# Performance work log

Hardware: AMD Instinct MI355X
Metric: run time of the kernel (lower is better)

The kernel has to match this reference:

```python
import jax, jax.numpy as jnp
import numpy as np

N, E, D, H = 100000, 400000, 128, 128  # nodes, edges, feat dim, mlp hidden


def _ln(x, g, b, eps=1e-5):
    m = jnp.mean(x, axis=-1, keepdims=True)
    v = jnp.mean((x - m) ** 2, axis=-1, keepdims=True)
    return (x - m) * jax.lax.rsqrt(v + eps) * g + b


def _mlp(x, w0, b0, w1, b1, w2, b2):
    # Linear->ReLU->Linear->ReLU->Linear (last act = Identity)
    h = jax.nn.relu(x @ w0 + b0)
    h = jax.nn.relu(h @ w1 + b1)
    return h @ w2 + b2


def setup_inputs() -> dict:
    key = jax.random.key(0)
    ks = jax.random.split(key, 16)
    node_x = jax.random.normal(ks[0], (N, D), dtype=jnp.float32)
    edge_attr = jax.random.normal(ks[1], (E, D), dtype=jnp.float32)
    edge_index = jax.random.randint(ks[2], (2, E), 0, N, dtype=jnp.int32)

    def lin(k, fin, fout):
        kw, kb = jax.random.split(k)
        s = 1.0 / np.sqrt(fin)
        w = jax.random.uniform(kw, (fin, fout), jnp.float32, -s, s)
        b = jax.random.uniform(kb, (fout,), jnp.float32, -s, s)
        return w, b

    # message MLP: (3D) -> H -> H -> D, then LayerNorm(D)
    msg_w0, msg_b0 = lin(ks[3], 3 * D, H)
    msg_w1, msg_b1 = lin(ks[4], H, H)
    msg_w2, msg_b2 = lin(ks[5], H, D)
    # top-level update MLP: (D + D) -> H -> H -> D, then LayerNorm(D)
    upd_w0, upd_b0 = lin(ks[6], 2 * D, H)
    upd_w1, upd_b1 = lin(ks[7], H, H)
    upd_w2, upd_b2 = lin(ks[8], H, D)
    return {
        "node_x": node_x, "edge_attr": edge_attr, "edge_index": edge_index,
        "msg_w0": msg_w0, "msg_b0": msg_b0, "msg_w1": msg_w1, "msg_b1": msg_b1,
        "msg_w2": msg_w2, "msg_b2": msg_b2,
        "msg_g": jnp.ones((D,), jnp.float32), "msg_beta": jnp.zeros((D,), jnp.float32),
        "upd_w0": upd_w0, "upd_b0": upd_b0, "upd_w1": upd_w1, "upd_b1": upd_b1,
        "upd_w2": upd_w2, "upd_b2": upd_b2,
        "upd_g": jnp.ones((D,), jnp.float32), "upd_beta": jnp.zeros((D,), jnp.float32),
    }


def reference(node_x, edge_attr, edge_index,
              msg_w0, msg_b0, msg_w1, msg_b1, msg_w2, msg_b2, msg_g, msg_beta,
              upd_w0, upd_b0, upd_w1, upd_b1, upd_w2, upd_b2, upd_g, upd_beta):
    src, dst = edge_index[0], edge_index[1]
    # PyG default flow source_to_target: x_j = x[src], x_i = x[dst]
    x_i = node_x[dst]                       # [E, D]
    x_j = node_x[src]                       # [E, D]
    concat = jnp.concatenate([x_i, x_j, edge_attr], axis=1)  # [E, 3D]
    msg = _ln(_mlp(concat, msg_w0, msg_b0, msg_w1, msg_b1, msg_w2, msg_b2), msg_g, msg_beta)
    new_edge = edge_attr + msg              # edge_attr[:] += msg in original
    # scatter-add messages onto target nodes
    agg = jax.ops.segment_sum(new_edge, dst, num_segments=N)  # [N, D]
    concat2 = jnp.concatenate([node_x, agg], axis=1)          # [N, 2D]
    upd = _ln(_mlp(concat2, upd_w0, upd_b0, upd_w1, upd_b1, upd_w2, upd_b2), upd_g, upd_beta)
    return node_x + upd
```

## Files before the change

### kernel.cpp

```cpp
#include <hip/hip_runtime.h>

typedef __attribute__((ext_vector_type(4))) float f32x4;
typedef __attribute__((ext_vector_type(8))) __bf16 bf16x8;

constexpr int FD = 128;

__device__ __forceinline__ uint4 pack8(const float* v) {
  union { __bf16 h[8]; uint4 u; } cv;
#pragma unroll
  for (int q = 0; q < 8; ++q) cv.h[q] = (__bf16)v[q];
  return cv.u;
}
__device__ __forceinline__ unsigned int pack2(float a, float b) {
  union { __bf16 h[2]; unsigned int u; } cv;
  cv.h[0] = (__bf16)a; cv.h[1] = (__bf16)b;
  return cv.u;
}

__global__ void cvt_bf16(const float* __restrict__ x, unsigned short* __restrict__ o, int n8) {
  int i = blockIdx.x * 256 + threadIdx.x;
  if (i >= n8) return;
  const float* p = x + (size_t)i * 8;
  float v[8];
#pragma unroll
  for (int q = 0; q < 8; ++q) v[q] = p[q];
  *(uint4*)(o + (size_t)i * 8) = pack8(v);
}

__global__ void pack_weights(const float* __restrict__ mw0, const float* __restrict__ mw1,
                             const float* __restrict__ mw2, const float* __restrict__ uw0,
                             const float* __restrict__ uw1, const float* __restrict__ uw2,
                             unsigned short* __restrict__ wp) {
  int tid = blockIdx.x * 256 + threadIdx.x;
  const float* src; int base, K;
  if      (tid < 49152)  { src = mw0; base = 0;      K = 384; }
  else if (tid < 65536)  { src = mw1; base = 49152;  K = 128; }
  else if (tid < 81920)  { src = mw2; base = 65536;  K = 128; }
  else if (tid < 114688) { src = uw0; base = 81920;  K = 256; }
  else if (tid < 131072) { src = uw1; base = 114688; K = 128; }
  else                   { src = uw2; base = 131072; K = 128; }
  int i = tid - base;
  int k = i >> 7, n = i & 127;
  int KS = K >> 5;
  int dst = base + (((n >> 4) * KS + (k >> 5)) * 64 + ((k >> 3) & 3) * 16 + (n & 15)) * 8 + (k & 7);
  union { __bf16 h; unsigned short s; } cv; cv.h = (__bf16)src[i];
  wp[dst] = cv.s;
}


template<bool RELU>
__device__ __forceinline__ void store_frag(unsigned short* sDst, const f32x4* acc, float bias) {
#pragma unroll
  for (int m = 0; m < 4; ++m)
#pragma unroll
    for (int ri = 0; ri < 4; ++ri) {
      float v = acc[m][ri] + bias;
      if (RELU) v = fmaxf(v, 0.f);
      union { __bf16 h; unsigned short s; } cv; cv.h = (__bf16)v;
      sDst[m * 512 + ri * 32] = cv.s;
    }
}

__global__ __launch_bounds__(512, 6)
void in_edge_kernel(const float* __restrict__ node_x, const unsigned short* __restrict__ nxbf,
                    const float* __restrict__ edge_attr,
                    const int* __restrict__ eidx, const unsigned short* __restrict__ wp,
                    const float* __restrict__ b0p, const float* __restrict__ b1p,
                    const float* __restrict__ b2p, const float* __restrict__ gp,
                    const float* __restrict__ bep,
                    unsigned short* __restrict__ msg, int* __restrict__ head,
                    int* __restrict__ nxt, float* __restrict__ agg,
                    int use_sort, int E) {
  __shared__ unsigned short sBuf[3072 * 8];
  __shared__ int sSrc[64], sDst[64];
  __shared__ float sG[128], sB[128];

  const int t = threadIdx.x;
  const int e0 = blockIdx.x * 64;
  const int lane = t & 63, w = t >> 6;
  const int ln = lane & 15, g16 = lane >> 4;
  const int col = w * 16 + ln;
  const int rdoff = ln * 32 + g16 * 8;
  const int stoff = (w >> 1) * 2048 + g16 * 128
                  + (((2 * w) + (ln >> 3)) & 3) * 8 + (ln & 7);

  bf16x8 b0[6];
#pragma unroll
  for (int ks = 0; ks < 6; ++ks)
    b0[ks] = *(const bf16x8*)(wp + (size_t)((w * 12 + ks) * 64 + lane) * 8);
  bf16x8 B1r[4];
#pragma unroll
  for (int ks = 0; ks < 4; ++ks)
    B1r[ks] = *(const bf16x8*)(wp + 49152 + (size_t)((w * 4 + ks) * 64 + lane) * 8);

  if (t < 64) {
    sSrc[t] = (e0 + t < E) ? eidx[e0 + t] : 0;
  } else if (t < 128) {
    int r = t - 64;
    int e = e0 + r;
    int d = (e < E) ? eidx[E + e] : 0;
    sDst[r] = d;
    if (use_sort && e < E) nxt[e] = atomicExch(&head[d], e);
  } else if (t < 256) {
    sG[t - 128] = gp[t - 128];
  } else if (t < 384) {
    sB[t - 256] = bep[t - 256];
  }
  __syncthreads();

  if (nxbf) {
#pragma unroll
    for (int it = 0; it < 2; ++it) {
      int f = t + it * 512;
      int row = f >> 4, j = f & 15;
      uint4 v = {0, 0, 0, 0}, u = {0, 0, 0, 0};
      if (e0 + row < E) {
        v = *(const uint4*)(nxbf + (size_t)sDst[row] * FD + j * 8);
        u = *(const uint4*)(nxbf + (size_t)sSrc[row] * FD + j * 8);
      }
      int c = (((j >> 2) * 4 + (row >> 4)) * 64 + (row & 15) * 4 + (j & 3)) * 8;
      *(uint4*)&sBuf[c] = v;
      *(uint4*)&sBuf[c + 8192] = u;
    }
  } else {
#pragma unroll
    for (int it = 0; it < 16; ++it) {
      const int type = it >> 3;
      int row = ((it & 7) << 3) + w;
      float2 v = {0.f, 0.f};
      if (e0 + row < E) {
        const float* sp = (type == 0) ? node_x + (size_t)sDst[row] * FD
                                      : node_x + (size_t)sSrc[row] * FD;
        v = *(const float2*)(sp + lane * 2);
      }
      int c = (((type * 4 + (lane >> 4)) * 4 + (row >> 4)) * 64
               + (row & 15) * 4 + ((lane >> 2) & 3)) * 8 + (lane & 3) * 2;
      *(unsigned int*)&sBuf[c] = pack2(v.x, v.y);
    }
  }
#pragma unroll
  for (int it = 0; it < 8; ++it) {
    int row = it * 8 + w;
    float2 v = {0.f, 0.f};
    if (e0 + row < E) v = *(const float2*)(edge_attr + (size_t)(e0 + row) * FD + lane * 2);
    int c = 16384 + (((lane >> 4) * 4 + (row >> 4)) * 64
                     + (row & 15) * 4 + ((lane >> 2) & 3)) * 8 + (lane & 3) * 2;
    *(unsigned int*)&sBuf[c] = pack2(v.x, v.y);
  }
  __syncthreads();

  const float b0v = b0p[col], b1v = b1p[col], b2v = b2p[col];

  f32x4 acc[4];
#pragma unroll
  for (int m = 0; m < 4; ++m) acc[m] = (f32x4){0.f, 0.f, 0.f, 0.f};

#pragma unroll
  for (int ks = 0; ks < 12; ++ks) {
    bf16x8 bb = b0[ks % 6];
    if (ks + 6 < 12)
      b0[ks % 6] = *(const bf16x8*)(wp + (size_t)((w * 12 + ks + 6) * 64 + lane) * 8);
#pragma unroll
    for (int m = 0; m < 4; ++m) {
      bf16x8 a = *(const bf16x8*)&sBuf[(ks * 4 + m) * 512 + rdoff];
      acc[m] = __builtin_amdgcn_mfma_f32_16x16x32_bf16(a, bb, acc[m], 0, 0, 0);
    }
  }
  bf16x8 B2r[4];
#pragma unroll
  for (int ks = 0; ks < 4; ++ks)
    B2r[ks] = *(const bf16x8*)(wp + 65536 + (size_t)((w * 4 + ks) * 64 + lane) * 8);

  __syncthreads();
  store_frag<true>(sBuf + stoff, acc, b0v);
  __syncthreads();

#pragma unroll
  for (int m = 0; m < 4; ++m) acc[m] = (f32x4){0.f, 0.f, 0.f, 0.f};
#pragma unroll
  for (int ks = 0; ks < 4; ++ks)
#pragma unroll
    for (int m = 0; m < 4; ++m) {
      bf16x8 a = *(const bf16x8*)&sBuf[(ks * 4 + m) * 512 + rdoff];
      acc[m] = __builtin_amdgcn_mfma_f32_16x16x32_bf16(a, B1r[ks], acc[m], 0, 0, 0);
    }
  store_frag<true>(sBuf + 8192 + stoff, acc, b1v);
  __syncthreads();

#pragma unroll
  for (int m = 0; m < 4; ++m) acc[m] = (f32x4){0.f, 0.f, 0.f, 0.f};
#pragma unroll
  for (int ks = 0; ks < 4; ++ks)
#pragma unroll
    for (int m = 0; m < 4; ++m) {
      bf16x8 a = *(const bf16x8*)&sBuf[8192 + (ks * 4 + m) * 512 + rdoff];
      acc[m] = __builtin_amdgcn_mfma_f32_16x16x32_bf16(a, B2r[ks], acc[m], 0, 0, 0);
    }
  store_frag<false>(sBuf + stoff, acc, b2v);
  __syncthreads();

  {
    int row = t >> 3, j = t & 7;
    int a0 = (((j >> 1) * 4 + (row >> 4)) * 64 + (row & 15) * 4 + 2 * (j & 1)) * 8;
    bf16x8 v0 = *(const bf16x8*)&sBuf[a0];
    bf16x8 v1 = *(const bf16x8*)&sBuf[a0 + 8];
    float s1 = 0.f, s2 = 0.f;
#pragma unroll
    for (int q = 0; q < 8; ++q) {
      float a = (float)v0[q], b = (float)v1[q];
      s1 += a + b; s2 += a * a + b * b;
    }
#pragma unroll
    for (int m = 1; m < 8; m <<= 1) {
      s1 += __shfl_xor(s1, m, 64);
      s2 += __shfl_xor(s2, m, 64);
    }
    float mean = s1 * (1.f / 128.f);
    float var  = s2 * (1.f / 128.f) - mean * mean;
    float rstd = rsqrtf(fmaxf(var, 0.f) + 1e-5f);

    int e = e0 + row;
    if (e < E) {
      bf16x8 ea0 = *(const bf16x8*)&sBuf[a0 + 16384];
      bf16x8 ea1 = *(const bf16x8*)&sBuf[a0 + 16384 + 8];
      float val[16];
#pragma unroll
      for (int q = 0; q < 8; ++q) {
        val[q]     = ((float)v0[q] - mean) * rstd * sG[j * 16 + q]     + sB[j * 16 + q]     + (float)ea0[q];
        val[8 + q] = ((float)v1[q] - mean) * rstd * sG[j * 16 + 8 + q] + sB[j * 16 + 8 + q] + (float)ea1[q];
      }
      if (use_sort) {
        uint4* dst = (uint4*)(msg + (size_t)e * FD + j * 16);
        dst[0] = pack8(val);
        dst[1] = pack8(val + 8);
      } else {
        float* ap = agg + (size_t)sDst[row] * FD + j * 16;
#pragma unroll
        for (int q = 0; q < 16; ++q) atomicAdd(ap + q, val[q]);
      }
    }
  }
}

__global__ __launch_bounds__(512, 8)
void in_node_kernel(const float* __restrict__ node_x, const unsigned short* __restrict__ nxbf,
                    const unsigned short* __restrict__ msg, const int* __restrict__ head,
                    const int* __restrict__ nxt, const float* __restrict__ agg,
                    const unsigned short* __restrict__ wp,
                    const float* __restrict__ b0p, const float* __restrict__ b1p,
                    const float* __restrict__ b2p, const float* __restrict__ gp,
                    const float* __restrict__ bep, float* __restrict__ out,
                    int use_sort, int N) {
  __shared__ unsigned short sBuf[2048 * 8];
  __shared__ float sG[128], sB[128];

  const int t = threadIdx.x;
  const int r0 = blockIdx.x * 64;
  const int lane = t & 63, w = t >> 6;
  const int ln = lane & 15, g16 = lane >> 4;
  const int col = w * 16 + ln;
  const int rdoff = ln * 32 + g16 * 8;
  const int stoff = (w >> 1) * 2048 + g16 * 128
                  + (((2 * w) + (ln >> 3)) & 3) * 8 + (ln & 7);

  bf16x8 b0[4];
#pragma unroll
  for (int ks = 0; ks < 4; ++ks)
    b0[ks] = *(const bf16x8*)(wp + 81920 + (size_t)((w * 8 + ks) * 64 + lane) * 8);

  if (t < 128)      sG[t] = gp[t];
  else if (t < 256) sB[t - 128] = bep[t - 128];

  if (nxbf) {
#pragma unroll
    for (int it = 0; it < 2; ++it) {
      int f = t + it * 512;
      int row = f >> 4, j = f & 15;
      int r = r0 + row;
      uint4 v = {0, 0, 0, 0};
      if (r < N) v = *(const uint4*)(nxbf + (size_t)r * FD + j * 8);
      int c = (((j >> 2) * 4 + (row >> 4)) * 64 + (row & 15) * 4 + (j & 3)) * 8;
      *(uint4*)&sBuf[c] = v;
    }
  } else {
#pragma unroll
    for (int it = 0; it < 8; ++it) {
      int row = (it << 3) + w;
      int r = r0 + row;
      float2 v = {0.f, 0.f};
      if (r < N) v = *(const float2*)(node_x + (size_t)r * FD + lane * 2);
      int c = (((lane >> 4) * 4 + (row >> 4)) * 64
               + (row & 15) * 4 + ((lane >> 2) & 3)) * 8 + (lane & 3) * 2;
      *(unsigned int*)&sBuf[c] = pack2(v.x, v.y);
    }
  }

  {
    int row = t >> 3, j = t & 7;
    int node = r0 + row;
    float a[16];
#pragma unroll
    for (int q = 0; q < 16; ++q) a[q] = 0.f;
    if (node < N) {
      if (use_sort) {
        int e = head[node];
        while (e >= 0) {
          int ne = nxt[e];
          bf16x8 m0 = *(const bf16x8*)(msg + (size_t)e * FD + j * 16);
          bf16x8 m1 = *(const bf16x8*)(msg + (size_t)e * FD + j * 16 + 8);
#pragma unroll
          for (int q = 0; q < 8; ++q) { a[q] += (float)m0[q]; a[8 + q] += (float)m1[q]; }
          e = ne;
        }
      } else {
        const float* ap = agg + (size_t)node * FD + j * 16;
#pragma unroll
        for (int q4 = 0; q4 < 4; ++q4) {
          f32x4 u = *(const f32x4*)(ap + q4 * 4);
#pragma unroll
          for (int q = 0; q < 4; ++q) a[q4 * 4 + q] = u[q];
        }
      }
    }
    int c = 8192 + (((j >> 1) * 4 + (row >> 4)) * 64 + (row & 15) * 4 + 2 * (j & 1)) * 8;
    *(uint4*)&sBuf[c] = pack8(a);
    *(uint4*)&sBuf[c + 8] = pack8(a + 8);
  }
  __syncthreads();

  const float b0v = b0p[col], b1v = b1p[col], b2v = b2p[col];

  f32x4 acc[4];
#pragma unroll
  for (int m = 0; m < 4; ++m) acc[m] = (f32x4){0.f, 0.f, 0.f, 0.f};

#pragma unroll
  for (int ks = 0; ks < 8; ++ks) {
    bf16x8 bb = b0[ks % 4];
    if (ks + 4 < 8)
      b0[ks % 4] = *(const bf16x8*)(wp + 81920 + (size_t)((w * 8 + ks + 4) * 64 + lane) * 8);
#pragma unroll
    for (int m = 0; m < 4; ++m) {
      bf16x8 a = *(const bf16x8*)&sBuf[(ks * 4 + m) * 512 + rdoff];
      acc[m] = __builtin_amdgcn_mfma_f32_16x16x32_bf16(a, bb, acc[m], 0, 0, 0);
    }
  }
  bf16x8 B1r[4];
#pragma unroll
  for (int ks = 0; ks < 4; ++ks)
    B1r[ks] = *(const bf16x8*)(wp + 114688 + (size_t)((w * 4 + ks) * 64 + lane) * 8);

  __syncthreads();
  store_frag<true>(sBuf + stoff, acc, b0v);
  __syncthreads();

#pragma unroll
  for (int m = 0; m < 4; ++m) acc[m] = (f32x4){0.f, 0.f, 0.f, 0.f};
#pragma unroll
  for (int ks = 0; ks < 4; ++ks)
#pragma unroll
    for (int m = 0; m < 4; ++m) {
      bf16x8 a = *(const bf16x8*)&sBuf[(ks * 4 + m) * 512 + rdoff];
      acc[m] = __builtin_amdgcn_mfma_f32_16x16x32_bf16(a, B1r[ks], acc[m], 0, 0, 0);
    }
  bf16x8 B2r[4];
#pragma unroll
  for (int ks = 0; ks < 4; ++ks)
    B2r[ks] = *(const bf16x8*)(wp + 131072 + (size_t)((w * 4 + ks) * 64 + lane) * 8);
  store_frag<true>(sBuf + 8192 + stoff, acc, b1v);
  __syncthreads();

#pragma unroll
  for (int m = 0; m < 4; ++m) acc[m] = (f32x4){0.f, 0.f, 0.f, 0.f};
#pragma unroll
  for (int ks = 0; ks < 4; ++ks)
#pragma unroll
    for (int m = 0; m < 4; ++m) {
      bf16x8 a = *(const bf16x8*)&sBuf[8192 + (ks * 4 + m) * 512 + rdoff];
      acc[m] = __builtin_amdgcn_mfma_f32_16x16x32_bf16(a, B2r[ks], acc[m], 0, 0, 0);
    }
  store_frag<false>(sBuf + stoff, acc, b2v);
  __syncthreads();

  {
    int row = t >> 3, j = t & 7;
    int a0 = (((j >> 1) * 4 + (row >> 4)) * 64 + (row & 15) * 4 + 2 * (j & 1)) * 8;
    bf16x8 v0 = *(const bf16x8*)&sBuf[a0];
    bf16x8 v1 = *(const bf16x8*)&sBuf[a0 + 8];
    float s1 = 0.f, s2 = 0.f;
#pragma unroll
    for (int q = 0; q < 8; ++q) {
      float a = (float)v0[q], b = (float)v1[q];
      s1 += a + b; s2 += a * a + b * b;
    }
#pragma unroll
    for (int m = 1; m < 8; m <<= 1) {
      s1 += __shfl_xor(s1, m, 64);
      s2 += __shfl_xor(s2, m, 64);
    }
    float mean = s1 * (1.f / 128.f);
    float var  = s2 * (1.f / 128.f) - mean * mean;
    float rstd = rsqrtf(fmaxf(var, 0.f) + 1e-5f);

    int node = r0 + row;
    if (node < N) {
      float o[16];
#pragma unroll
      for (int q = 0; q < 8; ++q) {
        o[q]     = ((float)v0[q] - mean) * rstd * sG[j * 16 + q]     + sB[j * 16 + q];
        o[8 + q] = ((float)v1[q] - mean) * rstd * sG[j * 16 + 8 + q] + sB[j * 16 + 8 + q];
      }
      const float* xr = node_x + (size_t)node * FD + j * 16;
      float* orow = out + (size_t)node * FD + j * 16;
#pragma unroll
      for (int q4 = 0; q4 < 4; ++q4) {
        f32x4 x = *(const f32x4*)(xr + q4 * 4);
        f32x4 wv;
#pragma unroll
        for (int q = 0; q < 4; ++q) wv[q] = o[q4 * 4 + q] + x[q];
        *(f32x4*)(orow + q4 * 4) = wv;
      }
    }
  }
}

extern "C" void kernel_launch(void* const* d_in, const int* in_sizes, int n_in,
                              void* d_out, int out_size, void* d_ws, size_t ws_size,
                              hipStream_t stream) {
  const float* node_x    = (const float*)d_in[0];
  const float* edge_attr = (const float*)d_in[1];
  const int*   eidx      = (const int*)d_in[2];
  const int N = in_sizes[0] / FD;
  const int E = in_sizes[1] / FD;

  char* ws = (char*)d_ws;
  auto aln = [](size_t x) { return (x + 255) & ~(size_t)255; };
  const size_t wpB   = aln(294912);
  const size_t nxbfB = aln((size_t)N * FD * 2);
  const size_t headB = aln((size_t)N * 4);
  const size_t nxtB  = aln((size_t)E * 4);
  const size_t msgB  = (size_t)E * FD * 2;

  unsigned short* wp = (unsigned short*)ws;
  unsigned short* nxbf = nullptr;
  int* head = nullptr; int* nxt = nullptr;
  unsigned short* msg = nullptr; float* agg = nullptr;
  int use_sort = 0;

  if (ws_size >= wpB + nxbfB + headB + nxtB + msgB) {
    use_sort = 1;
    nxbf = (unsigned short*)(ws + wpB);
    head = (int*)(ws + wpB + nxbfB);
    nxt  = (int*)(ws + wpB + nxbfB + headB);
    msg  = (unsigned short*)(ws + wpB + nxbfB + headB + nxtB);
  } else if (ws_size >= wpB + headB + nxtB + msgB) {
    use_sort = 1;
    head = (int*)(ws + wpB);
    nxt  = (int*)(ws + wpB + headB);
    msg  = (unsigned short*)(ws + wpB + headB + nxtB);
  } else {
    agg = (float*)(ws + wpB);
  }

  if (use_sort) (void)hipMemsetAsync(head, 0xFF, (size_t)N * 4, stream);
  else          (void)hipMemsetAsync(agg, 0, (size_t)N * FD * sizeof(float), stream);

  pack_weights<<<576, 256, 0, stream>>>(
      (const float*)d_in[3], (const float*)d_in[5], (const float*)d_in[7],
      (const float*)d_in[11], (const float*)d_in[13], (const float*)d_in[15], wp);
  if (nxbf) cvt_bf16<<<(N * FD / 8 + 255) / 256, 256, 0, stream>>>(node_x, nxbf, N * FD / 8);
  in_edge_kernel<<<(E + 63) / 64, 512, 0, stream>>>(
      node_x, nxbf, edge_attr, eidx, wp,
      (const float*)d_in[4], (const float*)d_in[6], (const float*)d_in[8],
      (const float*)d_in[9], (const float*)d_in[10],
      msg, head, nxt, agg, use_sort, E);
  in_node_kernel<<<(N + 63) / 64, 512, 0, stream>>>(
      node_x, nxbf, msg, head, nxt, agg, wp,
      (const float*)d_in[12], (const float*)d_in[14], (const float*)d_in[16],
      (const float*)d_in[17], (const float*)d_in[18], (float*)d_out, use_sort, N);
}
```

Before: 239.4 us.

## Process two edge tiles per block and prefetch second tile's gather during MLP

Each edge-kernel block now handles 128 edges as two 64-edge tiles. The node-feature gather for the second tile is issued into registers while the first tile's MLP runs, then written to shared memory after the first tile finishes. Weight register usage is trimmed from 6+4 to 4+4 buffers, reusing the first-layer buffer for the third layer. This overlaps gather latency with compute and amortizes setup, but doubles the per-block work, halves the grid, and adds register pressure from the prefetch buffers.

```diff
diff --git a/kernel.cpp b/kernel.cpp
--- a/kernel.cpp
+++ b/kernel.cpp
@@ -72,11 +72,11 @@
                     int* __restrict__ nxt, float* __restrict__ agg,
                     int use_sort, int E) {
   __shared__ unsigned short sBuf[3072 * 8];
-  __shared__ int sSrc[64], sDst[64];
+  __shared__ int sSrc[2][64], sDst[2][64];
   __shared__ float sG[128], sB[128];
 
   const int t = threadIdx.x;
-  const int e0 = blockIdx.x * 64;
+  const int e00 = blockIdx.x * 128;
   const int lane = t & 63, w = t >> 6;
   const int ln = lane & 15, g16 = lane >> 4;
   const int col = w * 16 + ln;
@@ -84,22 +84,73 @@
   const int stoff = (w >> 1) * 2048 + g16 * 128
                   + (((2 * w) + (ln >> 3)) & 3) * 8 + (ln & 7);
 
-  bf16x8 b0[6];
-#pragma unroll
-  for (int ks = 0; ks < 6; ++ks)
-    b0[ks] = *(const bf16x8*)(wp + (size_t)((w * 12 + ks) * 64 + lane) * 8);
-  bf16x8 B1r[4];
-#pragma unroll
-  for (int ks = 0; ks < 4; ++ks)
-    B1r[ks] = *(const bf16x8*)(wp + 49152 + (size_t)((w * 4 + ks) * 64 + lane) * 8);
+  bf16x8 bx[4], B1r[4];
+#pragma unroll
+  for (int k = 0; k < 4; ++k)
+    bx[k] = *(const bf16x8*)(wp + (size_t)((w * 12 + k) * 64 + lane) * 8);
+#pragma unroll
+  for (int k = 0; k < 4; ++k)
+    B1r[k] = *(const bf16x8*)(wp + 49152 + (size_t)((w * 4 + k) * 64 + lane) * 8);
+
+  uint4 pfv[2], pfu[2];
+
+  auto gatherX = [&](int eb, const int (&S)[64], const int (&D)[64]) {
+#pragma unroll
+    for (int it = 0; it < 2; ++it) {
+      int f = t + it * 512;
+      int row = f >> 4, j = f & 15;
+      uint4 v = {0, 0, 0, 0}, u = {0, 0, 0, 0};
+      if (eb + row < E) {
+        v = *(const uint4*)(nxbf + (size_t)D[row] * FD + j * 8);
+        u = *(const uint4*)(nxbf + (size_t)S[row] * FD + j * 8);
+      }
+      pfv[it] = v; pfu[it] = u;
+    }
+  };
+  auto writeX = [&]() {
+#pragma unroll
+    for (int it = 0; it < 2; ++it) {
+      int f = t + it * 512;
+      int row = f >> 4, j = f & 15;
+      int c = (((j >> 2) * 4 + (row >> 4)) * 64 + (row & 15) * 4 + (j & 3)) * 8;
+      *(uint4*)&sBuf[c] = pfv[it];
+      *(uint4*)&sBuf[c + 8192] = pfu[it];
+    }
+  };
+  auto stageXf32 = [&](int eb, const int (&S)[64], const int (&D)[64]) {
+#pragma unroll
+    for (int it = 0; it < 16; ++it) {
+      const int type = it >> 3;
+      int row = ((it & 7) << 3) + w;
+      float2 v = {0.f, 0.f};
+      if (eb + row < E) {
+        const float* sp = (type == 0) ? node_x + (size_t)D[row] * FD
+                                      : node_x + (size_t)S[row] * FD;
+        v = *(const float2*)(sp + lane * 2);
+      }
+      int c = (((type * 4 + (lane >> 4)) * 4 + (row >> 4)) * 64
+               + (row & 15) * 4 + ((lane >> 2) & 3)) * 8 + (lane & 3) * 2;
+      *(unsigned int*)&sBuf[c] = pack2(v.x, v.y);
+    }
+  };
+  auto stageEA = [&](int eb) {
+#pragma unroll
+    for (int it = 0; it < 8; ++it) {
+      int row = it * 8 + w;
+      float2 v = {0.f, 0.f};
+      if (eb + row < E) v = *(const float2*)(edge_attr + (size_t)(eb + row) * FD + lane * 2);
+      int c = 16384 + (((lane >> 4) * 4 + (row >> 4)) * 64
+                       + (row & 15) * 4 + ((lane >> 2) & 3)) * 8 + (lane & 3) * 2;
+      *(unsigned int*)&sBuf[c] = pack2(v.x, v.y);
+    }
+  };
 
   if (t < 64) {
-    sSrc[t] = (e0 + t < E) ? eidx[e0 + t] : 0;
+    sSrc[0][t] = (e00 + t < E) ? eidx[e00 + t] : 0;
   } else if (t < 128) {
-    int r = t - 64;
-    int e = e0 + r;
+    int r = t - 64, e = e00 + r;
     int d = (e < E) ? eidx[E + e] : 0;
-    sDst[r] = d;
+    sDst[0][r] = d;
     if (use_sort && e < E) nxt[e] = atomicExch(&head[d], e);
   } else if (t < 256) {
     sG[t - 128] = gp[t - 128];
@@ -108,136 +159,124 @@
   }
   __syncthreads();
 
-  if (nxbf) {
-#pragma unroll
-    for (int it = 0; it < 2; ++it) {
-      int f = t + it * 512;
-      int row = f >> 4, j = f & 15;
-      uint4 v = {0, 0, 0, 0}, u = {0, 0, 0, 0};
-      if (e0 + row < E) {
-        v = *(const uint4*)(nxbf + (size_t)sDst[row] * FD + j * 8);
-        u = *(const uint4*)(nxbf + (size_t)sSrc[row] * FD + j * 8);
-      }
-      int c = (((j >> 2) * 4 + (row >> 4)) * 64 + (row & 15) * 4 + (j & 3)) * 8;
-      *(uint4*)&sBuf[c] = v;
-      *(uint4*)&sBuf[c + 8192] = u;
-    }
-  } else {
-#pragma unroll
-    for (int it = 0; it < 16; ++it) {
-      const int type = it >> 3;
-      int row = ((it & 7) << 3) + w;
-      float2 v = {0.f, 0.f};
-      if (e0 + row < E) {
-        const float* sp = (type == 0) ? node_x + (size_t)sDst[row] * FD
-                                      : node_x + (size_t)sSrc[row] * FD;
-        v = *(const float2*)(sp + lane * 2);
-      }
-      int c = (((type * 4 + (lane >> 4)) * 4 + (row >> 4)) * 64
-               + (row & 15) * 4 + ((lane >> 2) & 3)) * 8 + (lane & 3) * 2;
-      *(unsigned int*)&sBuf[c] = pack2(v.x, v.y);
-    }
-  }
-#pragma unroll
-  for (int it = 0; it < 8; ++it) {
-    int row = it * 8 + w;
-    float2 v = {0.f, 0.f};
-    if (e0 + row < E) v = *(const float2*)(edge_attr + (size_t)(e0 + row) * FD + lane * 2);
-    int c = 16384 + (((lane >> 4) * 4 + (row >> 4)) * 64
-                     + (row & 15) * 4 + ((lane >> 2) & 3)) * 8 + (lane & 3) * 2;
-    *(unsigned int*)&sBuf[c] = pack2(v.x, v.y);
-  }
-  __syncthreads();
+  if (nxbf) { gatherX(e00, sSrc[0], sDst[0]); writeX(); }
+  else      stageXf32(e00, sSrc[0], sDst[0]);
+  stageEA(e00);
 
   const float b0v = b0p[col], b1v = b1p[col], b2v = b2p[col];
 
-  f32x4 acc[4];
-#pragma unroll
-  for (int m = 0; m < 4; ++m) acc[m] = (f32x4){0.f, 0.f, 0.f, 0.f};
-
-#pragma unroll
-  for (int ks = 0; ks < 12; ++ks) {
-    bf16x8 bb = b0[ks % 6];
-    if (ks + 6 < 12)
-      b0[ks % 6] = *(const bf16x8*)(wp + (size_t)((w * 12 + ks + 6) * 64 + lane) * 8);
-#pragma unroll
-    for (int m = 0; m < 4; ++m) {
-      bf16x8 a = *(const bf16x8*)&sBuf[(ks * 4 + m) * 512 + rdoff];
-      acc[m] = __builtin_amdgcn_mfma_f32_16x16x32_bf16(a, bb, acc[m], 0, 0, 0);
-    }
-  }
-  bf16x8 B2r[4];
-#pragma unroll
-  for (int ks = 0; ks < 4; ++ks)
-    B2r[ks] = *(const bf16x8*)(wp + 65536 + (size_t)((w * 4 + ks) * 64 + lane) * 8);
-
-  __syncthreads();
-  store_frag<true>(sBuf + stoff, acc, b0v);
-  __syncthreads();
-
-#pragma unroll
-  for (int m = 0; m < 4; ++m) acc[m] = (f32x4){0.f, 0.f, 0.f, 0.f};
-#pragma unroll
-  for (int ks = 0; ks < 4; ++ks)
-#pragma unroll
-    for (int m = 0; m < 4; ++m) {
-      bf16x8 a = *(const bf16x8*)&sBuf[(ks * 4 + m) * 512 + rdoff];
-      acc[m] = __builtin_amdgcn_mfma_f32_16x16x32_bf16(a, B1r[ks], acc[m], 0, 0, 0);
-    }
-  store_frag<true>(sBuf + 8192 + stoff, acc, b1v);
-  __syncthreads();
-
-#pragma unroll
-  for (int m = 0; m < 4; ++m) acc[m] = (f32x4){0.f, 0.f, 0.f, 0.f};
-#pragma unroll
-  for (int ks = 0; ks < 4; ++ks)
-#pragma unroll
-    for (int m = 0; m < 4; ++m) {
-      bf16x8 a = *(const bf16x8*)&sBuf[8192 + (ks * 4 + m) * 512 + rdoff];
-      acc[m] = __builtin_amdgcn_mfma_f32_16x16x32_bf16(a, B2r[ks], acc[m], 0, 0, 0);
-    }
-  store_frag<false>(sBuf + stoff, acc, b2v);
-  __syncthreads();
-
-  {
-    int row = t >> 3, j = t & 7;
-    int a0 = (((j >> 1) * 4 + (row >> 4)) * 64 + (row & 15) * 4 + 2 * (j & 1)) * 8;
-    bf16x8 v0 = *(const bf16x8*)&sBuf[a0];
-    bf16x8 v1 = *(const bf16x8*)&sBuf[a0 + 8];
-    float s1 = 0.f, s2 = 0.f;
-#pragma unroll
-    for (int q = 0; q < 8; ++q) {
-      float a = (float)v0[q], b = (float)v1[q];
-      s1 += a + b; s2 += a * a + b * b;
-    }
-#pragma unroll
-    for (int m = 1; m < 8; m <<= 1) {
-      s1 += __shfl_xor(s1, m, 64);
-      s2 += __shfl_xor(s2, m, 64);
-    }
-    float mean = s1 * (1.f / 128.f);
-    float var  = s2 * (1.f / 128.f) - mean * mean;
-    float rstd = rsqrtf(fmaxf(var, 0.f) + 1e-5f);
-
-    int e = e0 + row;
-    if (e < E) {
-      bf16x8 ea0 = *(const bf16x8*)&sBuf[a0 + 16384];
-      bf16x8 ea1 = *(const bf16x8*)&sBuf[a0 + 16384 + 8];
-      float val[16];
+#pragma unroll
+  for (int tile = 0; tile < 2; ++tile) {
+    const int e0 = e00 + tile * 64;
+    __syncthreads();
+    if (tile == 0) {
+      if (t < 64) {
+        sSrc[1][t] = (e00 + 64 + t < E) ? eidx[e00 + 64 + t] : 0;
+      } else if (t < 128) {
+        int r = t - 64, e = e00 + 64 + r;
+        int d = (e < E) ? eidx[E + e] : 0;
+        sDst[1][r] = d;
+        if (use_sort && e < E) nxt[e] = atomicExch(&head[d], e);
+      }
+    }
+
+    f32x4 acc[4];
+#pragma unroll
+    for (int m = 0; m < 4; ++m) acc[m] = (f32x4){0.f, 0.f, 0.f, 0.f};
+
+#pragma unroll
+    for (int ks = 0; ks < 12; ++ks) {
+      bf16x8 bb = bx[ks & 3];
+      if (ks + 4 < 12)
+        bx[ks & 3] = *(const bf16x8*)(wp + (size_t)((w * 12 + ks + 4) * 64 + lane) * 8);
+#pragma unroll
+      for (int m = 0; m < 4; ++m) {
+        bf16x8 a = *(const bf16x8*)&sBuf[(ks * 4 + m) * 512 + rdoff];
+        acc[m] = __builtin_amdgcn_mfma_f32_16x16x32_bf16(a, bb, acc[m], 0, 0, 0);
+      }
+    }
+    __syncthreads();
+    if (nxbf && tile == 0) gatherX(e00 + 64, sSrc[1], sDst[1]);
+#pragma unroll
+    for (int k = 0; k < 4; ++k)
+      bx[k] = *(const bf16x8*)(wp + 65536 + (size_t)((w * 4 + k) * 64 + lane) * 8);
+    store_frag<true>(sBuf + stoff, acc, b0v);
+    __syncthreads();
+
+#pragma unroll
+    for (int m = 0; m < 4; ++m) acc[m] = (f32x4){0.f, 0.f, 0.f, 0.f};
+#pragma unroll
+    for (int ks = 0; ks < 4; ++ks)
+#pragma unroll
+      for (int m = 0; m < 4; ++m) {
+        bf16x8 a = *(const bf16x8*)&sBuf[(ks * 4 + m) * 512 + rdoff];
+        acc[m] = __builtin_amdgcn_mfma_f32_16x16x32_bf16(a, B1r[ks], acc[m], 0, 0, 0);
+      }
+    store_frag<true>(sBuf + 8192 + stoff, acc, b1v);
+    __syncthreads();
+
+#pragma unroll
+    for (int m = 0; m < 4; ++m) acc[m] = (f32x4){0.f, 0.f, 0.f, 0.f};
+#pragma unroll
+    for (int ks = 0; ks < 4; ++ks)
+#pragma unroll
+      for (int m = 0; m < 4; ++m) {
+        bf16x8 a = *(const bf16x8*)&sBuf[8192 + (ks * 4 + m) * 512 + rdoff];
+        acc[m] = __builtin_amdgcn_mfma_f32_16x16x32_bf16(a, bx[ks], acc[m], 0, 0, 0);
+      }
+    store_frag<false>(sBuf + stoff, acc, b2v);
+    __syncthreads();
+
+    {
+      int row = t >> 3, j = t & 7;
+      int a0 = (((j >> 1) * 4 + (row >> 4)) * 64 + (row & 15) * 4 + 2 * (j & 1)) * 8;
+      bf16x8 v0 = *(const bf16x8*)&sBuf[a0];
+      bf16x8 v1 = *(const bf16x8*)&sBuf[a0 + 8];
+      float s1 = 0.f, s2 = 0.f;
 #pragma unroll
       for (int q = 0; q < 8; ++q) {
-        val[q]     = ((float)v0[q] - mean) * rstd * sG[j * 16 + q]     + sB[j * 16 + q]     + (float)ea0[q];
-        val[8 + q] = ((float)v1[q] - mean) * rstd * sG[j * 16 + 8 + q] + sB[j * 16 + 8 + q] + (float)ea1[q];
-      }
-      if (use_sort) {
-        uint4* dst = (uint4*)(msg + (size_t)e * FD + j * 16);
-        dst[0] = pack8(val);
-        dst[1] = pack8(val + 8);
-      } else {
-        float* ap = agg + (size_t)sDst[row] * FD + j * 16;
-#pragma unroll
-        for (int q = 0; q < 16; ++q) atomicAdd(ap + q, val[q]);
-      }
+        float a = (float)v0[q], b = (float)v1[q];
+        s1 += a + b; s2 += a * a + b * b;
+      }
+#pragma unroll
+      for (int m = 1; m < 8; m <<= 1) {
+        s1 += __shfl_xor(s1, m, 64);
+        s2 += __shfl_xor(s2, m, 64);
+      }
+      float mean = s1 * (1.f / 128.f);
+      float var  = s2 * (1.f / 128.f) - mean * mean;
+      float rstd = rsqrtf(fmaxf(var, 0.f) + 1e-5f);
+
+      int e = e0 + row;
+      if (e < E) {
+        bf16x8 ea0 = *(const bf16x8*)&sBuf[a0 + 16384];
+        bf16x8 ea1 = *(const bf16x8*)&sBuf[a0 + 16384 + 8];
+        float val[16];
+#pragma unroll
+        for (int q = 0; q < 8; ++q) {
+          val[q]     = ((float)v0[q] - mean) * rstd * sG[j * 16 + q]     + sB[j * 16 + q]     + (float)ea0[q];
+          val[8 + q] = ((float)v1[q] - mean) * rstd * sG[j * 16 + 8 + q] + sB[j * 16 + 8 + q] + (float)ea1[q];
+        }
+        if (use_sort) {
+          uint4* dst = (uint4*)(msg + (size_t)e * FD + j * 16);
+          dst[0] = pack8(val);
+          dst[1] = pack8(val + 8);
+        } else {
+          float* ap = agg + (size_t)sDst[tile][row] * FD + j * 16;
+#pragma unroll
+          for (int q = 0; q < 16; ++q) atomicAdd(ap + q, val[q]);
+        }
+      }
+    }
+
+    if (tile == 0) {
+      __syncthreads();
+      if (nxbf) writeX();
+      else      stageXf32(e00 + 64, sSrc[1], sDst[1]);
+      stageEA(e00 + 64);
+#pragma unroll
+      for (int k = 0; k < 4; ++k)
+        bx[k] = *(const bf16x8*)(wp + (size_t)((w * 12 + k) * 64 + lane) * 8);
     }
   }
 }
@@ -469,7 +508,7 @@
       (const float*)d_in[3], (const float*)d_in[5], (const float*)d_in[7],
       (const float*)d_in[11], (const float*)d_in[13], (const float*)d_in[15], wp);
   if (nxbf) cvt_bf16<<<(N * FD / 8 + 255) / 256, 256, 0, stream>>>(node_x, nxbf, N * FD / 8);
-  in_edge_kernel<<<(E + 63) / 64, 512, 0, stream>>>(
+  in_edge_kernel<<<(E + 127) / 128, 512, 0, stream>>>(
       node_x, nxbf, edge_attr, eidx, wp,
       (const float*)d_in[4], (const float*)d_in[6], (const float*)d_in[8],
       (const float*)d_in[9], (const float*)d_in[10],
```

Result: slower. 399.1 us (+66.7%).

## Retile edge MLP warps into 2x2 row/column blocks to reuse A fragments

Applied to the files above, without the earlier changes.

Each of the eight waves in the edge-message MLP used to own one 16-column slice across all 64 rows. Now each wave owns 32 rows by 32 columns, issuing two MFMAs per loaded A fragment instead of one. This halves the LDS reads of activations per wave, at the cost of loading twice as many B fragments per k-step. The first-layer weight prefetch depth drops from 6 to 4 k-steps, and the store_frag helper is inlined in both kernels with accumulator zeroing folded into the store loop.

```diff
diff --git a/kernel.cpp b/kernel.cpp
--- a/kernel.cpp
+++ b/kernel.cpp
@@ -48,19 +48,6 @@
 }
 
 
-template<bool RELU>
-__device__ __forceinline__ void store_frag(unsigned short* sDst, const f32x4* acc, float bias) {
-#pragma unroll
-  for (int m = 0; m < 4; ++m)
-#pragma unroll
-    for (int ri = 0; ri < 4; ++ri) {
-      float v = acc[m][ri] + bias;
-      if (RELU) v = fmaxf(v, 0.f);
-      union { __bf16 h; unsigned short s; } cv; cv.h = (__bf16)v;
-      sDst[m * 512 + ri * 32] = cv.s;
-    }
-}
-
 __global__ __launch_bounds__(512, 6)
 void in_edge_kernel(const float* __restrict__ node_x, const unsigned short* __restrict__ nxbf,
                     const float* __restrict__ edge_attr,
@@ -79,19 +66,20 @@
   const int e0 = blockIdx.x * 64;
   const int lane = t & 63, w = t >> 6;
   const int ln = lane & 15, g16 = lane >> 4;
-  const int col = w * 16 + ln;
+  const int rg = w & 1;
+  const int cg = w >> 1;
+  const int nt0 = cg * 2, nt1 = cg * 2 + 1;
   const int rdoff = ln * 32 + g16 * 8;
-  const int stoff = (w >> 1) * 2048 + g16 * 128
-                  + (((2 * w) + (ln >> 3)) & 3) * 8 + (ln & 7);
-
-  bf16x8 b0[6];
-#pragma unroll
-  for (int ks = 0; ks < 6; ++ks)
-    b0[ks] = *(const bf16x8*)(wp + (size_t)((w * 12 + ks) * 64 + lane) * 8);
-  bf16x8 B1r[4];
-#pragma unroll
-  for (int ks = 0; ks < 4; ++ks)
-    B1r[ks] = *(const bf16x8*)(wp + 49152 + (size_t)((w * 4 + ks) * 64 + lane) * 8);
+  const int stf = cg * 2048 + g16 * 128 + (ln & 7);
+  const int perm0 = (((ln >> 3)) & 3) * 8;
+  const int perm1 = ((2 + (ln >> 3)) & 3) * 8;
+
+  bf16x8 BA[8];
+#pragma unroll
+  for (int k = 0; k < 4; ++k) {
+    BA[k]     = *(const bf16x8*)(wp + (size_t)((nt0 * 12 + k) * 64 + lane) * 8);
+    BA[4 + k] = *(const bf16x8*)(wp + (size_t)((nt1 * 12 + k) * 64 + lane) * 8);
+  }
 
   if (t < 64) {
     sSrc[t] = (e0 + t < E) ? eidx[e0 + t] : 0;
@@ -149,54 +137,98 @@
   }
   __syncthreads();
 
-  const float b0v = b0p[col], b1v = b1p[col], b2v = b2p[col];
-
-  f32x4 acc[4];
-#pragma unroll
-  for (int m = 0; m < 4; ++m) acc[m] = (f32x4){0.f, 0.f, 0.f, 0.f};
+  const float b0A = b0p[cg * 32 + ln],      b0B = b0p[cg * 32 + 16 + ln];
+  const float b1A = b1p[cg * 32 + ln],      b1B = b1p[cg * 32 + 16 + ln];
+  const float b2A = b2p[cg * 32 + ln],      b2B = b2p[cg * 32 + 16 + ln];
+
+  f32x4 acc[2][2];
+#pragma unroll
+  for (int mi = 0; mi < 2; ++mi)
+#pragma unroll
+    for (int nj = 0; nj < 2; ++nj) acc[mi][nj] = (f32x4){0.f, 0.f, 0.f, 0.f};
 
 #pragma unroll
   for (int ks = 0; ks < 12; ++ks) {
-    bf16x8 bb = b0[ks % 6];
-    if (ks + 6 < 12)
-      b0[ks % 6] = *(const bf16x8*)(wp + (size_t)((w * 12 + ks + 6) * 64 + lane) * 8);
-#pragma unroll
-    for (int m = 0; m < 4; ++m) {
-      bf16x8 a = *(const bf16x8*)&sBuf[(ks * 4 + m) * 512 + rdoff];
-      acc[m] = __builtin_amdgcn_mfma_f32_16x16x32_bf16(a, bb, acc[m], 0, 0, 0);
-    }
-  }
-  bf16x8 B2r[4];
-#pragma unroll
-  for (int ks = 0; ks < 4; ++ks)
-    B2r[ks] = *(const bf16x8*)(wp + 65536 + (size_t)((w * 4 + ks) * 64 + lane) * 8);
-
-  __syncthreads();
-  store_frag<true>(sBuf + stoff, acc, b0v);
-  __syncthreads();
-
-#pragma unroll
-  for (int m = 0; m < 4; ++m) acc[m] = (f32x4){0.f, 0.f, 0.f, 0.f};
-#pragma unroll
-  for (int ks = 0; ks < 4; ++ks)
-#pragma unroll
-    for (int m = 0; m < 4; ++m) {
-      bf16x8 a = *(const bf16x8*)&sBuf[(ks * 4 + m) * 512 + rdoff];
-      acc[m] = __builtin_amdgcn_mfma_f32_16x16x32_bf16(a, B1r[ks], acc[m], 0, 0, 0);
-    }
-  store_frag<true>(sBuf + 8192 + stoff, acc, b1v);
-  __syncthreads();
-
-#pragma unroll
-  for (int m = 0; m < 4; ++m) acc[m] = (f32x4){0.f, 0.f, 0.f, 0.f};
-#pragma unroll
-  for (int ks = 0; ks < 4; ++ks)
-#pragma unroll
-    for (int m = 0; m < 4; ++m) {
-      bf16x8 a = *(const bf16x8*)&sBuf[8192 + (ks * 4 + m) * 512 + rdoff];
-      acc[m] = __builtin_amdgcn_mfma_f32_16x16x32_bf16(a, B2r[ks], acc[m], 0, 0, 0);
-    }
-  store_frag<false>(sBuf + stoff, acc, b2v);
+    bf16x8 bbA = BA[ks & 3];
+    bf16x8 bbB = BA[4 + (ks & 3)];
+    if (ks + 4 < 12) {
+      BA[ks & 3]       = *(const bf16x8*)(wp + (size_t)((nt0 * 12 + ks + 4) * 64 + lane) * 8);
+      BA[4 + (ks & 3)] = *(const bf16x8*)(wp + (size_t)((nt1 * 12 + ks + 4) * 64 + lane) * 8);
+    }
+#pragma unroll
+    for (int mi = 0; mi < 2; ++mi) {
+      bf16x8 a = *(const bf16x8*)&sBuf[(ks * 4 + rg * 2 + mi) * 512 + rdoff];
+      acc[mi][0] = __builtin_amdgcn_mfma_f32_16x16x32_bf16(a, bbA, acc[mi][0], 0, 0, 0);
+      acc[mi][1] = __builtin_amdgcn_mfma_f32_16x16x32_bf16(a, bbB, acc[mi][1], 0, 0, 0);
+    }
+  }
+#pragma unroll
+  for (int k = 0; k < 4; ++k) {
+    BA[k]     = *(const bf16x8*)(wp + 49152 + (size_t)((nt0 * 4 + k) * 64 + lane) * 8);
+    BA[4 + k] = *(const bf16x8*)(wp + 49152 + (size_t)((nt1 * 4 + k) * 64 + lane) * 8);
+  }
+  __syncthreads();
+
+#pragma unroll
+  for (int mi = 0; mi < 2; ++mi)
+#pragma unroll
+    for (int ri = 0; ri < 4; ++ri) {
+      union { __bf16 h; unsigned short s; } c0, c1;
+      c0.h = (__bf16)fmaxf(acc[mi][0][ri] + b0A, 0.f);
+      c1.h = (__bf16)fmaxf(acc[mi][1][ri] + b0B, 0.f);
+      int o = (rg * 2 + mi) * 512 + ri * 32 + stf;
+      sBuf[o + perm0] = c0.s;
+      sBuf[o + perm1] = c1.s;
+      acc[mi][0][ri] = 0.f; acc[mi][1][ri] = 0.f;
+    }
+  __syncthreads();
+
+#pragma unroll
+  for (int ks = 0; ks < 4; ++ks)
+#pragma unroll
+    for (int mi = 0; mi < 2; ++mi) {
+      bf16x8 a = *(const bf16x8*)&sBuf[(ks * 4 + rg * 2 + mi) * 512 + rdoff];
+      acc[mi][0] = __builtin_amdgcn_mfma_f32_16x16x32_bf16(a, BA[ks], acc[mi][0], 0, 0, 0);
+      acc[mi][1] = __builtin_amdgcn_mfma_f32_16x16x32_bf16(a, BA[4 + ks], acc[mi][1], 0, 0, 0);
+    }
+#pragma unroll
+  for (int k = 0; k < 4; ++k) {
+    BA[k]     = *(const bf16x8*)(wp + 65536 + (size_t)((nt0 * 4 + k) * 64 + lane) * 8);
+    BA[4 + k] = *(const bf16x8*)(wp + 65536 + (size_t)((nt1 * 4 + k) * 64 + lane) * 8);
+  }
+#pragma unroll
+  for (int mi = 0; mi < 2; ++mi)
+#pragma unroll
+    for (int ri = 0; ri < 4; ++ri) {
+      union { __bf16 h; unsigned short s; } c0, c1;
+      c0.h = (__bf16)fmaxf(acc[mi][0][ri] + b1A, 0.f);
+      c1.h = (__bf16)fmaxf(acc[mi][1][ri] + b1B, 0.f);
+      int o = 8192 + (rg * 2 + mi) * 512 + ri * 32 + stf;
+      sBuf[o + perm0] = c0.s;
+      sBuf[o + perm1] = c1.s;
+      acc[mi][0][ri] = 0.f; acc[mi][1][ri] = 0.f;
+    }
+  __syncthreads();
+
+#pragma unroll
+  for (int ks = 0; ks < 4; ++ks)
+#pragma unroll
+    for (int mi = 0; mi < 2; ++mi) {
+      bf16x8 a = *(const bf16x8*)&sBuf[8192 + (ks * 4 + rg * 2 + mi) * 512 + rdoff];
+      acc[mi][0] = __builtin_amdgcn_mfma_f32_16x16x32_bf16(a, BA[ks], acc[mi][0], 0, 0, 0);
+      acc[mi][1] = __builtin_amdgcn_mfma_f32_16x16x32_bf16(a, BA[4 + ks], acc[mi][1], 0, 0, 0);
+    }
+#pragma unroll
+  for (int mi = 0; mi < 2; ++mi)
+#pragma unroll
+    for (int ri = 0; ri < 4; ++ri) {
+      union { __bf16 h; unsigned short s; } c0, c1;
+      c0.h = (__bf16)(acc[mi][0][ri] + b2A);
+      c1.h = (__bf16)(acc[mi][1][ri] + b2B);
+      int o = (rg * 2 + mi) * 512 + ri * 32 + stf;
+      sBuf[o + perm0] = c0.s;
+      sBuf[o + perm1] = c1.s;
+    }
   __syncthreads();
 
   {
@@ -351,11 +383,17 @@
     B1r[ks] = *(const bf16x8*)(wp + 114688 + (size_t)((w * 4 + ks) * 64 + lane) * 8);
 
   __syncthreads();
-  store_frag<true>(sBuf + stoff, acc, b0v);
-  __syncthreads();
-
-#pragma unroll
-  for (int m = 0; m < 4; ++m) acc[m] = (f32x4){0.f, 0.f, 0.f, 0.f};
+#pragma unroll
+  for (int m = 0; m < 4; ++m)
+#pragma unroll
+    for (int ri = 0; ri < 4; ++ri) {
+      union { __bf16 h; unsigned short s; } cv;
+      cv.h = (__bf16)fmaxf(acc[m][ri] + b0v, 0.f);
+      sBuf[stoff + m * 512 + ri * 32] = cv.s;
+      acc[m][ri] = 0.f;
+    }
+  __syncthreads();
+
 #pragma unroll
   for (int ks = 0; ks < 4; ++ks)
 #pragma unroll
@@ -367,11 +405,17 @@
 #pragma unroll
   for (int ks = 0; ks < 4; ++ks)
     B2r[ks] = *(const bf16x8*)(wp + 131072 + (size_t)((w * 4 + ks) * 64 + lane) * 8);
-  store_frag<true>(sBuf + 8192 + stoff, acc, b1v);
-  __syncthreads();
-
-#pragma unroll
-  for (int m = 0; m < 4; ++m) acc[m] = (f32x4){0.f, 0.f, 0.f, 0.f};
+#pragma unroll
+  for (int m = 0; m < 4; ++m)
+#pragma unroll
+    for (int ri = 0; ri < 4; ++ri) {
+      union { __bf16 h; unsigned short s; } cv;
+      cv.h = (__bf16)fmaxf(acc[m][ri] + b1v, 0.f);
+      sBuf[8192 + stoff + m * 512 + ri * 32] = cv.s;
+      acc[m][ri] = 0.f;
+    }
+  __syncthreads();
+
 #pragma unroll
   for (int ks = 0; ks < 4; ++ks)
 #pragma unroll
@@ -379,7 +423,14 @@
       bf16x8 a = *(const bf16x8*)&sBuf[8192 + (ks * 4 + m) * 512 + rdoff];
       acc[m] = __builtin_amdgcn_mfma_f32_16x16x32_bf16(a, B2r[ks], acc[m], 0, 0, 0);
     }
-  store_frag<false>(sBuf + stoff, acc, b2v);
+#pragma unroll
+  for (int m = 0; m < 4; ++m)
+#pragma unroll
+    for (int ri = 0; ri < 4; ++ri) {
+      union { __bf16 h; unsigned short s; } cv;
+      cv.h = (__bf16)(acc[m][ri] + b2v);
+      sBuf[stoff + m * 512 + ri * 32] = cv.s;
+    }
   __syncthreads();
 
   {
```

Result: slower. 245.0 us (+2.3%).
